# Optimization experiments

Measured on AMD Instinct MI355X. Metric: run time of the kernel, lower is better.

The kernel has to match this reference:

```python
import jax, jax.numpy as jnp
import numpy as np

B, T, I, H = 512, 64, 128, 128
E = I - 1  # encoder_in


def _cell(x, h, c, Wih, Whh, bih, bhh):
    # PyTorch LSTM gate order: i, f, g, o
    g = x @ Wih.T + h @ Whh.T + bih + bhh
    i, f, gg, o = jnp.split(g, 4, axis=-1)
    c2 = jax.nn.sigmoid(f) * c + jax.nn.sigmoid(i) * jnp.tanh(gg)
    h2 = jax.nn.sigmoid(o) * jnp.tanh(c2)
    return h2, c2


def setup_inputs() -> dict:
    key = jax.random.key(0)
    ks = iter(jax.random.split(key, 40))
    n = lambda *s: jax.random.normal(next(ks), s, dtype=jnp.float32) * 0.05
    inp = {
        'input_data': jax.random.normal(next(ks), (B, T, I), dtype=jnp.float32),
        # encoder LSTM (2 layers, input E)
        'enc_Wih0': n(4 * H, E), 'enc_Whh0': n(4 * H, H), 'enc_bih0': n(4 * H), 'enc_bhh0': n(4 * H),
        'enc_Wih1': n(4 * H, H), 'enc_Whh1': n(4 * H, H), 'enc_bih1': n(4 * H), 'enc_bhh1': n(4 * H),
        # decoder LSTM (2 layers, input 1)
        'dec_Wih0': n(4 * H, 1), 'dec_Whh0': n(4 * H, H), 'dec_bih0': n(4 * H), 'dec_bhh0': n(4 * H),
        'dec_Wih1': n(4 * H, H), 'dec_Whh1': n(4 * H, H), 'dec_bih1': n(4 * H), 'dec_bhh1': n(4 * H),
        # input attention MLP: (2H+T)->T->1
        'attn_W1': n(T, 2 * H + T), 'attn_b1': n(T), 'attn_W2': n(1, T), 'attn_b2': n(1),
        # temporal attention MLP: 3H->H->1
        'attnd_W1': n(H, 3 * H), 'attnd_b1': n(H), 'attnd_W2': n(1, H), 'attnd_b2': n(1),
        # decoder input projection (H+1)->1 and output projection 2H->1
        'decin_W': n(1, H + 1), 'decin_b': n(1),
        'proj_W': n(1, 2 * H), 'proj_b': n(1),
    }
    return inp


def reference(input_data, enc_Wih0, enc_Whh0, enc_bih0, enc_bhh0,
              enc_Wih1, enc_Whh1, enc_bih1, enc_bhh1,
              dec_Wih0, dec_Whh0, dec_bih0, dec_bhh0,
              dec_Wih1, dec_Whh1, dec_bih1, dec_bhh1,
              attn_W1, attn_b1, attn_W2, attn_b2,
              attnd_W1, attnd_b1, attnd_W2, attnd_b2,
              decin_W, decin_b, proj_W, proj_b):
    b, t, i = input_data.shape
    e, hdim = i - 1, enc_Whh0.shape[1]
    inp_enc = input_data[:, :, 1:]              # [B,T,E]
    inp_dec = input_data[:, :, 0]               # [B,T]
    inp_perm = jnp.transpose(inp_enc, (0, 2, 1))  # [B,E,T]
    z = jnp.zeros((b, hdim), input_data.dtype)

    def enc_step(carry, x_t):
        h0, c0, h1, c1 = carry
        hc = jnp.concatenate([
            jnp.broadcast_to(h1[:, None, :], (b, e, hdim)),
            jnp.broadcast_to(c1[:, None, :], (b, e, hdim)),
            inp_perm], axis=-1)                              # [B,E,2H+T]
        logits = jnp.tanh(hc @ attn_W1.T + attn_b1) @ attn_W2.T + attn_b2
        a = jax.nn.softmax(logits[..., 0], axis=-1)          # [B,E]
        h0, c0 = _cell(x_t * a, h0, c0, enc_Wih0, enc_Whh0, enc_bih0, enc_bhh0)
        h1, c1 = _cell(h0, h1, c1, enc_Wih1, enc_Whh1, enc_bih1, enc_bhh1)
        return (h0, c0, h1, c1), h1

    _, h_top = jax.lax.scan(enc_step, (z, z, z, z), jnp.transpose(inp_enc, (1, 0, 2)))
    h_exp = jnp.transpose(h_top, (1, 0, 2))  # [B,T,H]

    def dec_step(carry, x_t):
        h0, c0, h1, c1, _ = carry
        hc = jnp.concatenate([
            jnp.broadcast_to(h1[:, None, :], (b, t, hdim)),
            jnp.broadcast_to(c1[:, None, :], (b, t, hdim)),
            h_exp], axis=-1)                                  # [B,T,3H]
        logits = jnp.tanh(hc @ attnd_W1.T + attnd_b1) @ attnd_W2.T + attnd_b2
        a = jax.nn.softmax(logits[..., 0], axis=-1)           # [B,T]
        partial = jnp.einsum('bth,bt->bh', h_exp, a)          # [B,H]
        full = jnp.concatenate([partial, x_t[:, None]], axis=-1)  # [B,H+1]
        din = full @ decin_W.T + decin_b                      # [B,1]
        h0, c0 = _cell(din, h0, c0, dec_Wih0, dec_Whh0, dec_bih0, dec_bhh0)
        h1, c1 = _cell(h0, h1, c1, dec_Wih1, dec_Whh1, dec_bih1, dec_bhh1)
        return (h0, c0, h1, c1, partial), None

    (h0, c0, h1, c1, partial), _ = jax.lax.scan(dec_step, (z, z, z, z, z), jnp.transpose(inp_dec))
    out = jnp.concatenate([h1, partial], axis=-1) @ proj_W.T + proj_b  # [B,1]
    return out
```

## Files before the change

### kernel.cpp

```cpp
#include <hip/hip_runtime.h>

#define BATCH 512
#define TT 64
#define II 128

#define OFF_Wr_e0 0
#define OFF_Wr_e1 (OFF_Wr_e0 + 512*256)
#define OFF_Wr_d1 (OFF_Wr_e1 + 512*256)
#define OFF_bs0e  (OFF_Wr_d1 + 512*256)
#define OFF_bs1e  (OFF_bs0e + 512)
#define OFF_bs0d  (OFF_bs1e + 512)
#define OFF_bs1d  (OFF_bs0d + 512)
#define OFF_xprojT (OFF_bs1d + 512)
#define OFF_hexp   (OFF_xprojT + BATCH*8192)
#define OFF_hprojT (OFF_hexp + BATCH*8192)

struct Params {
  const float* input;
  const float *eWih0, *eWhh0, *ebih0, *ebhh0, *eWih1, *eWhh1, *ebih1, *ebhh1;
  const float *dWih0, *dWhh0, *dbih0, *dbhh0, *dWih1, *dWhh1, *dbih1, *dbhh1;
  const float *aW1, *ab1, *aW2, *ab2;
  const float *adW1, *adb1, *adW2, *adb2;
  const float *dinW, *dinb, *projW, *projb;
  float* ws;
  float* out;
};

#define L2E 1.4426950408889634f

__device__ __forceinline__ float exp2f_(float x){ return __builtin_amdgcn_exp2f(x); }
__device__ __forceinline__ float rcp_(float x){ return __builtin_amdgcn_rcpf(x); }
__device__ __forceinline__ float fast_tanh(float x){
  float t = exp2f_(x * 2.8853900817779268f);
  return 1.f - 2.f * rcp_(t + 1.f);
}
__device__ __forceinline__ float sigm(float x){
  return rcp_(1.f + exp2f_(-x * L2E));
}
__device__ __forceinline__ float wave_max(float v){
  #pragma unroll
  for (int o = 32; o > 0; o >>= 1) v = fmaxf(v, __shfl_xor(v, o, 64));
  return v;
}
__device__ __forceinline__ float wave_sum(float v){
  #pragma unroll
  for (int o = 32; o > 0; o >>= 1) v += __shfl_xor(v, o, 64);
  return v;
}

__global__ __launch_bounds__(256) void k_prep(Params p){
  float* ws = p.ws;
  const int gid = blockIdx.x*256 + threadIdx.x;
  const int gsz = gridDim.x*256;
  for (int i = gid; i < 512*256; i += gsz){
    const int j = i >> 8, k = i & 255;
    ws[OFF_Wr_e0 + i] = (k < 128) ? ((k < 127) ? p.eWih0[j*127 + k] : 0.f)
                                  : p.eWhh0[j*128 + (k-128)];
    ws[OFF_Wr_e1 + i] = (k < 128) ? p.eWih1[j*128 + k] : p.eWhh1[j*128 + (k-128)];
    ws[OFF_Wr_d1 + i] = (k < 128) ? p.dWih1[j*128 + k] : p.dWhh1[j*128 + (k-128)];
  }
  for (int i = gid; i < 512; i += gsz){
    ws[OFF_bs0e+i] = p.ebih0[i]+p.ebhh0[i];
    ws[OFF_bs1e+i] = p.ebih1[i]+p.ebhh1[i];
    ws[OFF_bs0d+i] = p.dbih0[i]+p.dbhh0[i];
    ws[OFF_bs1d+i] = p.dbih1[i]+p.dbhh1[i];
  }
}

__global__ __launch_bounds__(256) void k_xproj(Params p){
  __shared__ float xin[64][128];
  __shared__ float w1x[64][64];
  __shared__ float b1s[64];
  const int b = blockIdx.x, tid = threadIdx.x;
  const float* inb = p.input + (size_t)b*(TT*II);
  for (int i = tid; i < 64*128; i += 256){
    const int k = i >> 7, e = i & 127;
    xin[k][e] = (e < 127) ? inb[k*II + 1 + e] : 0.f;
  }
  for (int i = tid; i < 64*64; i += 256){
    const int j = i >> 6, k = i & 63;
    w1x[j][k] = p.aW1[j*320 + 256 + k];
  }
  if (tid < 64) b1s[tid] = p.ab1[tid];
  __syncthreads();
  float* outb = p.ws + OFF_xprojT + (size_t)b*8192;
  for (int i = tid; i < 64*128; i += 256){
    const int j = i >> 7, e = i & 127;
    float acc = b1s[j];
    #pragma unroll 8
    for (int k = 0; k < 64; ++k) acc += xin[k][e] * w1x[j][k];
    outb[i] = acc;
  }
}

__global__ __launch_bounds__(256) void k_hproj(Params p){
  __shared__ float hx[64][129];
  __shared__ float bs[128];
  const int b = blockIdx.x, tid = threadIdx.x;
  const float* hb = p.ws + OFF_hexp + (size_t)b*8192;
  for (int i = tid; i < 64*128; i += 256){
    hx[i>>7][i&127] = hb[i];
  }
  if (tid < 128) bs[tid] = p.adb1[tid];
  __syncthreads();
  float* outb = p.ws + OFF_hprojT + (size_t)b*8192;
  for (int i = tid; i < 128*64; i += 256){
    const int kk = i >> 6, t2 = i & 63;
    const float* w = p.adW1 + kk*384 + 256;
    float acc = bs[kk];
    #pragma unroll 8
    for (int k = 0; k < 128; ++k) acc += hx[t2][k] * w[k];
    outb[i] = acc;
  }
}

#define ENC_LDS_FLOATS 40784
__global__ __launch_bounds__(1024, 4) void k_enc(Params p){
  extern __shared__ float sm[];
  float* xp  = sm;
  float* Se  = xp + 32768;
  float* c0  = Se + 2048;
  float* gpA = c0 + 512;
  float* gpB = gpA + 2048;
  float* scr = gpB + 2048;
  float* g01 = scr + 1024;
  float* w2  = g01 + 256;
  float* pm  = w2 + 64;
  float* psu = pm + 8;
  const int tid = threadIdx.x;
  const int b0 = blockIdx.x * 4;
  float* ws = p.ws;

  {
    const float4* xsrc = (const float4*)(ws + OFF_xprojT + (size_t)b0*8192);
    float4* xdst = (float4*)xp;
    for (int i = tid; i < 8192; i += 1024) xdst[i] = xsrc[i];
  }
  for (int i = tid; i < 2048; i += 1024) Se[i] = 0.f;
  if (tid < 512) c0[tid] = 0.f;
  if (tid < 64) w2[tid] = p.aW2[tid];
  const float b2 = p.ab2[0];
  const int j = tid & 511, kh = tid >> 9;
  const float bias0 = ws[OFF_bs0e + j];
  const float bias1 = ws[OFF_bs1e + j];
  const int jj = tid & 63, bb1 = (tid>>6)&3, kq = tid >> 8;
  const int e2 = tid & 127, bb2 = (tid>>7)&3, jh = tid >> 9;
  const int hf = (tid>>6)&1;
  __syncthreads();

  for (int t = 0; t < TT; ++t){
    {
      const float4* wr = (const float4*)(p.aW1 + jj*320 + kq*64);
      const float4* s1 = (const float4*)(Se + bb1*512 + 256 + kq*64);
      float a = 0.f;
      #pragma unroll 8
      for (int g = 0; g < 16; ++g){
        const float4 w = wr[g], x = s1[g];
        a += w.x*x.x + w.y*x.y + w.z*x.z + w.w*x.w;
      }
      scr[kq*256 + bb1*64 + jj] = a;
    }
    __syncthreads();
    if (tid < 256) g01[tid] = scr[tid] + scr[256+tid] + scr[512+tid] + scr[768+tid];
    __syncthreads();
    {
      const float* xpe = xp + bb2*8192 + e2;
      const float* gg = g01 + bb2*64 + jh*32;
      const float* w2p = w2 + jh*32;
      float acc = 0.f;
      #pragma unroll 8
      for (int q = 0; q < 32; ++q)
        acc += w2p[q] * fast_tanh(xpe[(jh*32+q)*128] + gg[q]);
      scr[jh*512 + bb2*128 + e2] = acc;
    }
    __syncthreads();
    float acc_l;
    {
      acc_l = scr[bb2*128 + e2] + scr[512 + bb2*128 + e2] + b2;
      if (e2 == 127) acc_l = -3.0e38f;
      const float m = wave_max(acc_l);
      const float pe = exp2f_((acc_l - m)*L2E);
      const float s = wave_sum(pe);
      if ((tid & 63) == 0){ pm[bb2*2+hf] = m; psu[bb2*2+hf] = s; }
    }
    __syncthreads();
    {
      const float m0 = pm[bb2*2], m1 = pm[bb2*2+1];
      const float gm = fmaxf(m0, m1);
      const float tot = psu[bb2*2]*exp2f_((m0-gm)*L2E) + psu[bb2*2+1]*exp2f_((m1-gm)*L2E);
      const float a = exp2f_((acc_l - gm)*L2E) * rcp_(tot);
      float xv = 0.f;
      if (e2 < 127) xv = p.input[(size_t)(b0+bb2)*8192 + t*128 + 1 + e2] * a;
      Se[bb2*512 + e2] = xv;
    }
    __syncthreads();
    {
      const float4* r  = (const float4*)(ws + OFF_Wr_e0 + (j<<8) + (kh<<7));
      const float4* x0 = (const float4*)(Se + (kh<<7));
      const float4* x1 = (const float4*)(Se + 512 + (kh<<7));
      const float4* x2 = (const float4*)(Se + 1024 + (kh<<7));
      const float4* x3 = (const float4*)(Se + 1536 + (kh<<7));
      float a0,a1,a2,a3; a0=a1=a2=a3 = kh ? 0.f : bias0;
      #pragma unroll 8
      for (int kg = 0; kg < 32; ++kg){
        const float4 w = r[kg];
        const float4 v0=x0[kg], v1=x1[kg], v2=x2[kg], v3=x3[kg];
        a0 += w.x*v0.x + w.y*v0.y + w.z*v0.z + w.w*v0.w;
        a1 += w.x*v1.x + w.y*v1.y + w.z*v1.z + w.w*v1.w;
        a2 += w.x*v2.x + w.y*v2.y + w.z*v2.z + w.w*v2.w;
        a3 += w.x*v3.x + w.y*v3.y + w.z*v3.z + w.w*v3.w;
      }
      float* gp = kh ? gpB : gpA;
      gp[j] = a0; gp[512+j] = a1; gp[1024+j] = a2; gp[1536+j] = a3;
    }
    __syncthreads();
    if (tid < 512){
      const int bb = tid>>7, u = tid&127;
      const float* gA = gpA + bb*512; const float* gB = gpB + bb*512;
      const float gi = gA[u]+gB[u], gf = gA[128+u]+gB[128+u];
      const float gg2 = gA[256+u]+gB[256+u], go = gA[384+u]+gB[384+u];
      const float c = sigm(gf)*c0[tid] + sigm(gi)*fast_tanh(gg2);
      c0[tid] = c;
      Se[bb*512 + 128 + u] = sigm(go)*fast_tanh(c);
    }
    __syncthreads();
    {
      const float4* r  = (const float4*)(ws + OFF_Wr_e1 + (j<<8) + (kh<<7));
      const float4* x0 = (const float4*)(Se + 128 + (kh<<7));
      const float4* x1 = (const float4*)(Se + 640 + (kh<<7));
      const float4* x2 = (const float4*)(Se + 1152 + (kh<<7));
      const float4* x3 = (const float4*)(Se + 1664 + (kh<<7));
      float a0,a1,a2,a3; a0=a1=a2=a3 = kh ? 0.f : bias1;
      #pragma unroll 8
      for (int kg = 0; kg < 32; ++kg){
        const float4 w = r[kg];
        const float4 v0=x0[kg], v1=x1[kg], v2=x2[kg], v3=x3[kg];
        a0 += w.x*v0.x + w.y*v0.y + w.z*v0.z + w.w*v0.w;
        a1 += w.x*v1.x + w.y*v1.y + w.z*v1.z + w.w*v1.w;
        a2 += w.x*v2.x + w.y*v2.y + w.z*v2.z + w.w*v2.w;
        a3 += w.x*v3.x + w.y*v3.y + w.z*v3.z + w.w*v3.w;
      }
      float* gp = kh ? gpB : gpA;
      gp[j] = a0; gp[512+j] = a1; gp[1024+j] = a2; gp[1536+j] = a3;
    }
    __syncthreads();
    if (tid < 512){
      const int bb = tid>>7, u = tid&127;
      const float* gA = gpA + bb*512; const float* gB = gpB + bb*512;
      const float gi = gA[u]+gB[u], gf = gA[128+u]+gB[128+u];
      const float gg2 = gA[256+u]+gB[256+u], go = gA[384+u]+gB[384+u];
      const float c = sigm(gf)*Se[bb*512+384+u] + sigm(gi)*fast_tanh(gg2);
      Se[bb*512+384+u] = c;
      const float h = sigm(go)*fast_tanh(c);
      Se[bb*512+256+u] = h;
      ws[OFF_hexp + (size_t)(b0+bb)*8192 + t*128 + u] = h;
    }
    __syncthreads();
  }
}

#define DEC_LDS_FLOATS 40584
__global__ __launch_bounds__(1024, 4) void k_dec(Params p){
  extern __shared__ float sm[];
  float* hp  = sm;
  float* Sd  = hp + 32768;
  float* c0  = Sd + 1536;
  float* gpA = c0 + 512;
  float* gpB = gpA + 2048;
  float* scr = gpB + 2048;
  float* g01 = scr + 1024;
  float* wd2 = g01 + 512;
  float* dins= wd2 + 128;
  const int tid = threadIdx.x;
  const int b0 = blockIdx.x * 4;
  float* ws = p.ws;

  {
    const float4* hsrc = (const float4*)(ws + OFF_hprojT + (size_t)b0*8192);
    float4* hdst = (float4*)hp;
    for (int i = tid; i < 8192; i += 1024) hdst[i] = hsrc[i];
  }
  for (int i = tid; i < 1536; i += 1024) Sd[i] = 0.f;
  if (tid < 512) c0[tid] = 0.f;
  if (tid < 128) wd2[tid] = p.adW2[tid];
  const int j = tid & 511, kh = tid >> 9;
  const float bias0d = ws[OFF_bs0d + j];
  const float bias1d = ws[OFF_bs1d + j];
  const float dW0j = p.dWih0[j];
  const int o = tid & 511, bbD = o>>7, kkD = o&127;
  const int l = tid & 63, wv = tid >> 6;
  const int bbA = wv>>2, kqA = wv&3;
  const int th = tid>>9, bbC = (tid>>7)&3, hC = tid&127;
  const float dinw0 = p.dinW[l], dinw1 = p.dinW[64+l];
  const float dinw128 = p.dinW[128], dinbv = p.dinb[0];
  const float bd2 = p.adb2[0];
  const float pw0 = p.projW[l], pw1 = p.projW[64+l];
  const float pw2 = p.projW[128+l], pw3 = p.projW[192+l];
  const float pb = p.projb[0];
  __syncthreads();

  for (int t = 0; t < TT; ++t){
    {
      const float4* wr = (const float4*)(p.adW1 + kkD*384 + (kh<<7));
      const float4* sx = (const float4*)(Sd + bbD*384 + 128 + (kh<<7));
      float a = 0.f;
      #pragma unroll 8
      for (int kg = 0; kg < 32; ++kg){
        const float4 w = wr[kg], x = sx[kg];
        a += w.x*x.x + w.y*x.y + w.z*x.z + w.w*x.w;
      }
      (kh ? gpB : gpA)[o] = a;
    }
    __syncthreads();
    g01[tid&511] = gpA[tid&511] + gpB[tid&511];
    __syncthreads();
    {
      const float* hpb = hp + bbA*8192 + l;
      const float* gg = g01 + bbA*128 + kqA*32;
      const float* w2p = wd2 + kqA*32;
      float acc = 0.f;
      #pragma unroll 8
      for (int q = 0; q < 32; ++q)
        acc += w2p[q] * fast_tanh(hpb[(kqA*32+q)*64] + gg[q]);
      scr[kqA*256 + bbA*64 + l] = acc;
    }
    __syncthreads();
    {
      const int q = tid & 255;
      float acc = scr[q] + scr[256+q] + scr[512+q] + scr[768+q] + bd2;
      const float m = wave_max(acc);
      const float pe = exp2f_((acc - m)*L2E);
      const float s = wave_sum(pe);
      g01[q] = pe * rcp_(s);
    }
    __syncthreads();
    {
      const float* he = ws + OFF_hexp + (size_t)(b0+bbC)*8192 + hC;
      const float* av = g01 + bbC*64 + th*32;
      float acc = 0.f;
      #pragma unroll 8
      for (int q = 0; q < 32; ++q)
        acc += av[q] * he[(th*32+q)*128];
      (th ? gpB : gpA)[bbC*128 + hC] = acc;
    }
    __syncthreads();
    scr[tid&511] = gpA[tid&511] + gpB[tid&511];
    __syncthreads();
    if (wv < 4){
      float v = scr[wv*128 + l]*dinw0 + scr[wv*128 + 64 + l]*dinw1;
      v = wave_sum(v);
      if (l == 0){
        const float xd = p.input[(size_t)(b0+wv)*8192 + t*128];
        dins[wv] = v + xd*dinw128 + dinbv;
      }
    }
    __syncthreads();
    {
      const float4* wr = (const float4*)(p.dWhh0 + (j<<7) + (kh<<6));
      const float4* x0 = (const float4*)(Sd + (kh<<6));
      const float4* x1 = (const float4*)(Sd + 384 + (kh<<6));
      const float4* x2 = (const float4*)(Sd + 768 + (kh<<6));
      const float4* x3 = (const float4*)(Sd + 1152 + (kh<<6));
      float a0,a1,a2,a3;
      if (kh){ a0=a1=a2=a3=0.f; }
      else {
        a0 = bias0d + dins[0]*dW0j; a1 = bias0d + dins[1]*dW0j;
        a2 = bias0d + dins[2]*dW0j; a3 = bias0d + dins[3]*dW0j;
      }
      #pragma unroll 8
      for (int kg = 0; kg < 16; ++kg){
        const float4 w = wr[kg];
        const float4 v0=x0[kg], v1=x1[kg], v2=x2[kg], v3=x3[kg];
        a0 += w.x*v0.x + w.y*v0.y + w.z*v0.z + w.w*v0.w;
        a1 += w.x*v1.x + w.y*v1.y + w.z*v1.z + w.w*v1.w;
        a2 += w.x*v2.x + w.y*v2.y + w.z*v2.z + w.w*v2.w;
        a3 += w.x*v3.x + w.y*v3.y + w.z*v3.z + w.w*v3.w;
      }
      float* gp = kh ? gpB : gpA;
      gp[j] = a0; gp[512+j] = a1; gp[1024+j] = a2; gp[1536+j] = a3;
    }
    __syncthreads();
    if (tid < 512){
      const int bb = tid>>7, u = tid&127;
      const float* gA = gpA + bb*512; const float* gB = gpB + bb*512;
      const float gi = gA[u]+gB[u], gf = gA[128+u]+gB[128+u];
      const float gg2 = gA[256+u]+gB[256+u], go = gA[384+u]+gB[384+u];
      const float c = sigm(gf)*c0[tid] + sigm(gi)*fast_tanh(gg2);
      c0[tid] = c;
      Sd[bb*384 + u] = sigm(go)*fast_tanh(c);
    }
    __syncthreads();
    {
      const float4* wr = (const float4*)(ws + OFF_Wr_d1 + (j<<8) + (kh<<7));
      const float4* x0 = (const float4*)(Sd + (kh<<7));
      const float4* x1 = (const float4*)(Sd + 384 + (kh<<7));
      const float4* x2 = (const float4*)(Sd + 768 + (kh<<7));
      const float4* x3 = (const float4*)(Sd + 1152 + (kh<<7));
      float a0,a1,a2,a3; a0=a1=a2=a3 = kh ? 0.f : bias1d;
      #pragma unroll 8
      for (int kg = 0; kg < 32; ++kg){
        const float4 w = wr[kg];
        const float4 v0=x0[kg], v1=x1[kg], v2=x2[kg], v3=x3[kg];
        a0 += w.x*v0.x + w.y*v0.y + w.z*v0.z + w.w*v0.w;
        a1 += w.x*v1.x + w.y*v1.y + w.z*v1.z + w.w*v1.w;
        a2 += w.x*v2.x + w.y*v2.y + w.z*v2.z + w.w*v2.w;
        a3 += w.x*v3.x + w.y*v3.y + w.z*v3.z + w.w*v3.w;
      }
      float* gp = kh ? gpB : gpA;
      gp[j] = a0; gp[512+j] = a1; gp[1024+j] = a2; gp[1536+j] = a3;
    }
    __syncthreads();
    if (tid < 512){
      const int bb = tid>>7, u = tid&127;
      const float* gA = gpA + bb*512; const float* gB = gpB + bb*512;
      const float gi = gA[u]+gB[u], gf = gA[128+u]+gB[128+u];
      const float gg2 = gA[256+u]+gB[256+u], go = gA[384+u]+gB[384+u];
      const float c = sigm(gf)*Sd[bb*384+256+u] + sigm(gi)*fast_tanh(gg2);
      Sd[bb*384+256+u] = c;
      Sd[bb*384+128+u] = sigm(go)*fast_tanh(c);
    }
    __syncthreads();
  }
  if (wv < 4){
    float v = Sd[wv*384+128+l]*pw0 + Sd[wv*384+192+l]*pw1
            + scr[wv*128+l]*pw2 + scr[wv*128+64+l]*pw3;
    v = wave_sum(v);
    if (l == 0) p.out[b0 + wv] = v + pb;
  }
}

extern "C" void kernel_launch(void* const* d_in, const int* in_sizes, int n_in,
                              void* d_out, int out_size, void* d_ws, size_t ws_size,
                              hipStream_t stream){
  Params p;
  p.input = (const float*)d_in[0];
  p.eWih0=(const float*)d_in[1];  p.eWhh0=(const float*)d_in[2];
  p.ebih0=(const float*)d_in[3];  p.ebhh0=(const float*)d_in[4];
  p.eWih1=(const float*)d_in[5];  p.eWhh1=(const float*)d_in[6];
  p.ebih1=(const float*)d_in[7];  p.ebhh1=(const float*)d_in[8];
  p.dWih0=(const float*)d_in[9];  p.dWhh0=(const float*)d_in[10];
  p.dbih0=(const float*)d_in[11]; p.dbhh0=(const float*)d_in[12];
  p.dWih1=(const float*)d_in[13]; p.dWhh1=(const float*)d_in[14];
  p.dbih1=(const float*)d_in[15]; p.dbhh1=(const float*)d_in[16];
  p.aW1=(const float*)d_in[17];   p.ab1=(const float*)d_in[18];
  p.aW2=(const float*)d_in[19];   p.ab2=(const float*)d_in[20];
  p.adW1=(const float*)d_in[21];  p.adb1=(const float*)d_in[22];
  p.adW2=(const float*)d_in[23];  p.adb2=(const float*)d_in[24];
  p.dinW=(const float*)d_in[25];  p.dinb=(const float*)d_in[26];
  p.projW=(const float*)d_in[27]; p.projb=(const float*)d_in[28];
  p.ws = (float*)d_ws;
  p.out = (float*)d_out;

  (void)hipFuncSetAttribute(reinterpret_cast<const void*>(k_enc),
      hipFuncAttributeMaxDynamicSharedMemorySize, ENC_LDS_FLOATS*4);
  (void)hipFuncSetAttribute(reinterpret_cast<const void*>(k_dec),
      hipFuncAttributeMaxDynamicSharedMemorySize, DEC_LDS_FLOATS*4);

  hipLaunchKernelGGL(k_prep,  dim3(128), dim3(256), 0, stream, p);
  hipLaunchKernelGGL(k_xproj, dim3(BATCH), dim3(256), 0, stream, p);
  hipLaunchKernelGGL(k_enc,   dim3(128), dim3(1024), ENC_LDS_FLOATS*4, stream, p);
  hipLaunchKernelGGL(k_hproj, dim3(BATCH), dim3(256), 0, stream, p);
  hipLaunchKernelGGL(k_dec,   dim3(128), dim3(1024), DEC_LDS_FLOATS*4, stream, p);
}
```

Baseline: 5.658 ms.

## Restructure encoder/decoder recurrence to cut barriers and reductions via wave shuffles

Thread-to-work mappings in the recurrent encoder and decoder kernels are remapped so partial dot-product sums are combined with intra-wave shuffles instead of LDS scratch passes. This removes several block-wide barriers per timestep. __syncthreads is replaced with a custom lgkmcnt wait plus s_barrier. The first weight vectors are prefetched into registers, the decoder's projected-history tile gets a padded LDS layout, and hexp is written with nontemporal stores. The cost is higher register pressure, and the custom barrier only waits on LDS and scalar-memory (lgkmcnt) operations, not on outstanding global loads.

New measurement: 5.655 ms. No clear change (-0.1%).

```diff
diff --git a/kernel.cpp b/kernel.cpp
--- a/kernel.cpp
+++ b/kernel.cpp
@@ -47,6 +47,15 @@
   for (int o = 32; o > 0; o >>= 1) v += __shfl_xor(v, o, 64);
   return v;
 }
+__device__ __forceinline__ void bar_lds(){
+  asm volatile("s_waitcnt lgkmcnt(0)\n\ts_barrier" ::: "memory");
+}
+
+#define FMA4(W,V0,V1,V2,V3) \
+  a0 += (W).x*(V0).x + (W).y*(V0).y + (W).z*(V0).z + (W).w*(V0).w; \
+  a1 += (W).x*(V1).x + (W).y*(V1).y + (W).z*(V1).z + (W).w*(V1).w; \
+  a2 += (W).x*(V2).x + (W).y*(V2).y + (W).z*(V2).z + (W).w*(V2).w; \
+  a3 += (W).x*(V3).x + (W).y*(V3).y + (W).z*(V3).z + (W).w*(V3).w;
 
 __global__ __launch_bounds__(256) void k_prep(Params p){
   float* ws = p.ws;
@@ -98,9 +107,7 @@
   __shared__ float bs[128];
   const int b = blockIdx.x, tid = threadIdx.x;
   const float* hb = p.ws + OFF_hexp + (size_t)b*8192;
-  for (int i = tid; i < 64*128; i += 256){
-    hx[i>>7][i&127] = hb[i];
-  }
+  for (int i = tid; i < 64*128; i += 256) hx[i>>7][i&127] = hb[i];
   if (tid < 128) bs[tid] = p.adb1[tid];
   __syncthreads();
   float* outb = p.ws + OFF_hprojT + (size_t)b*8192;
@@ -114,318 +121,313 @@
   }
 }
 
-#define ENC_LDS_FLOATS 40784
+#define ENC_LDS_FLOATS 39776
 __global__ __launch_bounds__(1024, 4) void k_enc(Params p){
   extern __shared__ float sm[];
-  float* xp  = sm;
-  float* Se  = xp + 32768;
-  float* c0  = Se + 2048;
-  float* gpA = c0 + 512;
-  float* gpB = gpA + 2048;
-  float* scr = gpB + 2048;
-  float* g01 = scr + 1024;
-  float* w2  = g01 + 256;
-  float* pm  = w2 + 64;
-  float* psu = pm + 8;
+  float* xp   = sm;
+  float* Se   = xp + 32768;
+  float* c0s  = Se + 2048;
+  float* gpA  = c0s + 512;
+  float* gpB  = gpA + 2048;
+  float* g01s = gpB + 2048;
+  float* w2   = g01s + 256;
+  float* pm   = w2 + 64;
+  float* psu  = pm + 16;
   const int tid = threadIdx.x;
-  const int b0 = blockIdx.x * 4;
+  const int b0 = blockIdx.x*4;
   float* ws = p.ws;
 
-  {
-    const float4* xsrc = (const float4*)(ws + OFF_xprojT + (size_t)b0*8192);
+  { const float4* xsrc = (const float4*)(ws + OFF_xprojT + (size_t)b0*8192);
     float4* xdst = (float4*)xp;
-    for (int i = tid; i < 8192; i += 1024) xdst[i] = xsrc[i];
-  }
+    for (int i = tid; i < 8192; i += 1024) xdst[i] = xsrc[i]; }
   for (int i = tid; i < 2048; i += 1024) Se[i] = 0.f;
-  if (tid < 512) c0[tid] = 0.f;
+  if (tid < 512) c0s[tid] = 0.f;
   if (tid < 64) w2[tid] = p.aW2[tid];
   const float b2 = p.ab2[0];
-  const int j = tid & 511, kh = tid >> 9;
-  const float bias0 = ws[OFF_bs0e + j];
-  const float bias1 = ws[OFF_bs1e + j];
-  const int jj = tid & 63, bb1 = (tid>>6)&3, kq = tid >> 8;
-  const int e2 = tid & 127, bb2 = (tid>>7)&3, jh = tid >> 9;
-  const int hf = (tid>>6)&1;
+
+  const int bbW = tid >> 8;
+  const int wvq = (tid >> 6) & 3;
+  const int kqE = tid & 3, oE = tid >> 2, jjE = oE & 63;
+  const int jhE = tid & 1, eE = (tid >> 1) & 127;
+  const int jG = tid & 511, khG = tid >> 9;
+  const float bias0 = ws[OFF_bs0e + jG];
+  const float bias1 = ws[OFF_bs1e + jG];
+  const float4* wE1 = (const float4*)(p.aW1 + jjE*320 + kqE*64);
+  const float4* wE3 = (const float4*)(ws + OFF_Wr_e0 + (jG<<8) + (khG<<7));
+  const float4* wE4 = (const float4*)(ws + OFF_Wr_e1 + (jG<<8) + (khG<<7));
+  const float* xrow = p.input + (size_t)(b0+bbW)*8192 + 1 + eE;
+  float4 pfE1[4], pfE3[4], pfE4[4];
+  #pragma unroll
+  for (int i = 0; i < 4; ++i){ pfE1[i]=wE1[i]; pfE3[i]=wE3[i]; pfE4[i]=wE4[i]; }
   __syncthreads();
 
   for (int t = 0; t < TT; ++t){
     {
-      const float4* wr = (const float4*)(p.aW1 + jj*320 + kq*64);
-      const float4* s1 = (const float4*)(Se + bb1*512 + 256 + kq*64);
+      const float4* s1 = (const float4*)(Se + bbW*512 + 256 + kqE*64);
+      float a = 0.f;
+      #pragma unroll
+      for (int kg = 0; kg < 4; ++kg){ float4 w = pfE1[kg], x = s1[kg];
+        a += w.x*x.x + w.y*x.y + w.z*x.z + w.w*x.w; }
+      #pragma unroll
+      for (int kg = 4; kg < 16; ++kg){ float4 w = wE1[kg], x = s1[kg];
+        a += w.x*x.x + w.y*x.y + w.z*x.z + w.w*x.w; }
+      a += __shfl_xor(a, 1, 64);
+      a += __shfl_xor(a, 2, 64);
+      if (kqE == 0) g01s[oE] = a;
+    }
+    bar_lds();
+    float accL;
+    {
+      const float* xpe = xp + bbW*8192 + eE;
+      const float* gg = g01s + bbW*64 + jhE*32;
+      const float* w2p = w2 + jhE*32;
       float a = 0.f;
       #pragma unroll 8
-      for (int g = 0; g < 16; ++g){
-        const float4 w = wr[g], x = s1[g];
-        a += w.x*x.x + w.y*x.y + w.z*x.z + w.w*x.w;
-      }
-      scr[kq*256 + bb1*64 + jj] = a;
-    }
-    __syncthreads();
-    if (tid < 256) g01[tid] = scr[tid] + scr[256+tid] + scr[512+tid] + scr[768+tid];
-    __syncthreads();
-    {
-      const float* xpe = xp + bb2*8192 + e2;
-      const float* gg = g01 + bb2*64 + jh*32;
-      const float* w2p = w2 + jh*32;
-      float acc = 0.f;
-      #pragma unroll 8
       for (int q = 0; q < 32; ++q)
-        acc += w2p[q] * fast_tanh(xpe[(jh*32+q)*128] + gg[q]);
-      scr[jh*512 + bb2*128 + e2] = acc;
-    }
-    __syncthreads();
-    float acc_l;
-    {
-      acc_l = scr[bb2*128 + e2] + scr[512 + bb2*128 + e2] + b2;
-      if (e2 == 127) acc_l = -3.0e38f;
-      const float m = wave_max(acc_l);
-      const float pe = exp2f_((acc_l - m)*L2E);
-      const float s = wave_sum(pe);
-      if ((tid & 63) == 0){ pm[bb2*2+hf] = m; psu[bb2*2+hf] = s; }
-    }
-    __syncthreads();
-    {
-      const float m0 = pm[bb2*2], m1 = pm[bb2*2+1];
-      const float gm = fmaxf(m0, m1);
-      const float tot = psu[bb2*2]*exp2f_((m0-gm)*L2E) + psu[bb2*2+1]*exp2f_((m1-gm)*L2E);
-      const float a = exp2f_((acc_l - gm)*L2E) * rcp_(tot);
+        a += w2p[q] * fast_tanh(xpe[(jhE*32+q)*128] + gg[q]);
+      a += __shfl_xor(a, 1, 64);
+      a += b2;
+      if (eE == 127) a = -3.0e38f;
+      accL = a;
+      const float m = wave_max(a);
+      const float pe = exp2f_((a - m)*L2E);
+      const float s = wave_sum(pe)*0.5f;
+      if ((tid & 63) == 0){ pm[bbW*4+wvq] = m; psu[bbW*4+wvq] = s; }
+    }
+    bar_lds();
+    {
+      const float m0=pm[bbW*4],m1=pm[bbW*4+1],m2=pm[bbW*4+2],m3=pm[bbW*4+3];
+      const float gm = fmaxf(fmaxf(m0,m1),fmaxf(m2,m3));
+      const float tot = psu[bbW*4]*exp2f_((m0-gm)*L2E) + psu[bbW*4+1]*exp2f_((m1-gm)*L2E)
+                      + psu[bbW*4+2]*exp2f_((m2-gm)*L2E) + psu[bbW*4+3]*exp2f_((m3-gm)*L2E);
+      const float a = exp2f_((accL-gm)*L2E)*rcp_(tot);
       float xv = 0.f;
-      if (e2 < 127) xv = p.input[(size_t)(b0+bb2)*8192 + t*128 + 1 + e2] * a;
-      Se[bb2*512 + e2] = xv;
-    }
-    __syncthreads();
-    {
-      const float4* r  = (const float4*)(ws + OFF_Wr_e0 + (j<<8) + (kh<<7));
-      const float4* x0 = (const float4*)(Se + (kh<<7));
-      const float4* x1 = (const float4*)(Se + 512 + (kh<<7));
-      const float4* x2 = (const float4*)(Se + 1024 + (kh<<7));
-      const float4* x3 = (const float4*)(Se + 1536 + (kh<<7));
-      float a0,a1,a2,a3; a0=a1=a2=a3 = kh ? 0.f : bias0;
-      #pragma unroll 8
-      for (int kg = 0; kg < 32; ++kg){
-        const float4 w = r[kg];
-        const float4 v0=x0[kg], v1=x1[kg], v2=x2[kg], v3=x3[kg];
-        a0 += w.x*v0.x + w.y*v0.y + w.z*v0.z + w.w*v0.w;
-        a1 += w.x*v1.x + w.y*v1.y + w.z*v1.z + w.w*v1.w;
-        a2 += w.x*v2.x + w.y*v2.y + w.z*v2.z + w.w*v2.w;
-        a3 += w.x*v3.x + w.y*v3.y + w.z*v3.z + w.w*v3.w;
-      }
-      float* gp = kh ? gpB : gpA;
-      gp[j] = a0; gp[512+j] = a1; gp[1024+j] = a2; gp[1536+j] = a3;
-    }
-    __syncthreads();
+      if (eE < 127) xv = xrow[t*128] * a;
+      Se[bbW*512 + eE] = xv;
+    }
+    bar_lds();
+    {
+      float a0,a1,a2,a3; a0=a1=a2=a3 = khG ? 0.f : bias0;
+      const float4* x0 = (const float4*)(Se + (khG<<7));
+      const float4* x1 = x0 + 128; const float4* x2 = x0 + 256; const float4* x3 = x0 + 384;
+      #pragma unroll
+      for (int kg = 0; kg < 4; ++kg){ float4 w = pfE3[kg];
+        float4 v0=x0[kg],v1=x1[kg],v2=x2[kg],v3=x3[kg]; FMA4(w,v0,v1,v2,v3) }
+      #pragma unroll 7
+      for (int kg = 4; kg < 32; ++kg){ float4 w = wE3[kg];
+        float4 v0=x0[kg],v1=x1[kg],v2=x2[kg],v3=x3[kg]; FMA4(w,v0,v1,v2,v3) }
+      float* gp = khG ? gpB : gpA;
+      gp[jG]=a0; gp[512+jG]=a1; gp[1024+jG]=a2; gp[1536+jG]=a3;
+    }
+    bar_lds();
     if (tid < 512){
       const int bb = tid>>7, u = tid&127;
       const float* gA = gpA + bb*512; const float* gB = gpB + bb*512;
-      const float gi = gA[u]+gB[u], gf = gA[128+u]+gB[128+u];
-      const float gg2 = gA[256+u]+gB[256+u], go = gA[384+u]+gB[384+u];
-      const float c = sigm(gf)*c0[tid] + sigm(gi)*fast_tanh(gg2);
-      c0[tid] = c;
+      const float gi=gA[u]+gB[u], gf=gA[128+u]+gB[128+u];
+      const float gg2=gA[256+u]+gB[256+u], go=gA[384+u]+gB[384+u];
+      const float c = sigm(gf)*c0s[tid] + sigm(gi)*fast_tanh(gg2);
+      c0s[tid] = c;
       Se[bb*512 + 128 + u] = sigm(go)*fast_tanh(c);
     }
-    __syncthreads();
-    {
-      const float4* r  = (const float4*)(ws + OFF_Wr_e1 + (j<<8) + (kh<<7));
-      const float4* x0 = (const float4*)(Se + 128 + (kh<<7));
-      const float4* x1 = (const float4*)(Se + 640 + (kh<<7));
-      const float4* x2 = (const float4*)(Se + 1152 + (kh<<7));
-      const float4* x3 = (const float4*)(Se + 1664 + (kh<<7));
-      float a0,a1,a2,a3; a0=a1=a2=a3 = kh ? 0.f : bias1;
-      #pragma unroll 8
-      for (int kg = 0; kg < 32; ++kg){
-        const float4 w = r[kg];
-        const float4 v0=x0[kg], v1=x1[kg], v2=x2[kg], v3=x3[kg];
-        a0 += w.x*v0.x + w.y*v0.y + w.z*v0.z + w.w*v0.w;
-        a1 += w.x*v1.x + w.y*v1.y + w.z*v1.z + w.w*v1.w;
-        a2 += w.x*v2.x + w.y*v2.y + w.z*v2.z + w.w*v2.w;
-        a3 += w.x*v3.x + w.y*v3.y + w.z*v3.z + w.w*v3.w;
-      }
-      float* gp = kh ? gpB : gpA;
-      gp[j] = a0; gp[512+j] = a1; gp[1024+j] = a2; gp[1536+j] = a3;
-    }
-    __syncthreads();
+    bar_lds();
+    {
+      float a0,a1,a2,a3; a0=a1=a2=a3 = khG ? 0.f : bias1;
+      const float4* x0 = (const float4*)(Se + 128 + (khG<<7));
+      const float4* x1 = x0 + 128; const float4* x2 = x0 + 256; const float4* x3 = x0 + 384;
+      #pragma unroll
+      for (int kg = 0; kg < 4; ++kg){ float4 w = pfE4[kg];
+        float4 v0=x0[kg],v1=x1[kg],v2=x2[kg],v3=x3[kg]; FMA4(w,v0,v1,v2,v3) }
+      #pragma unroll 7
+      for (int kg = 4; kg < 32; ++kg){ float4 w = wE4[kg];
+        float4 v0=x0[kg],v1=x1[kg],v2=x2[kg],v3=x3[kg]; FMA4(w,v0,v1,v2,v3) }
+      float* gp = khG ? gpB : gpA;
+      gp[jG]=a0; gp[512+jG]=a1; gp[1024+jG]=a2; gp[1536+jG]=a3;
+    }
+    bar_lds();
     if (tid < 512){
       const int bb = tid>>7, u = tid&127;
       const float* gA = gpA + bb*512; const float* gB = gpB + bb*512;
-      const float gi = gA[u]+gB[u], gf = gA[128+u]+gB[128+u];
-      const float gg2 = gA[256+u]+gB[256+u], go = gA[384+u]+gB[384+u];
+      const float gi=gA[u]+gB[u], gf=gA[128+u]+gB[128+u];
+      const float gg2=gA[256+u]+gB[256+u], go=gA[384+u]+gB[384+u];
       const float c = sigm(gf)*Se[bb*512+384+u] + sigm(gi)*fast_tanh(gg2);
       Se[bb*512+384+u] = c;
       const float h = sigm(go)*fast_tanh(c);
       Se[bb*512+256+u] = h;
-      ws[OFF_hexp + (size_t)(b0+bb)*8192 + t*128 + u] = h;
-    }
-    __syncthreads();
-  }
-}
-
-#define DEC_LDS_FLOATS 40584
+      __builtin_nontemporal_store(h, ws + OFF_hexp + (size_t)(b0+bb)*8192 + t*128 + u);
+    }
+    bar_lds();
+  }
+}
+
+#define DEC_LDS_FLOATS 40880
 __global__ __launch_bounds__(1024, 4) void k_dec(Params p){
   extern __shared__ float sm[];
-  float* hp  = sm;
-  float* Sd  = hp + 32768;
-  float* c0  = Sd + 1536;
-  float* gpA = c0 + 512;
-  float* gpB = gpA + 2048;
-  float* scr = gpB + 2048;
-  float* g01 = scr + 1024;
-  float* wd2 = g01 + 512;
-  float* dins= wd2 + 128;
+  float* hp    = sm;
+  float* Sd    = hp + 33280;
+  float* c0s   = Sd + 1536;
+  float* gpA   = c0s + 512;
+  float* gpB   = gpA + 2048;
+  float* parts = gpB + 2048;
+  float* g01d  = parts + 512;
+  float* lraw  = g01d + 512;
+  float* pm    = lraw + 256;
+  float* psu   = pm + 16;
+  float* dpart = psu + 16;
+  float* wd2   = dpart + 16;
   const int tid = threadIdx.x;
-  const int b0 = blockIdx.x * 4;
+  const int b0 = blockIdx.x*4;
   float* ws = p.ws;
 
-  {
-    const float4* hsrc = (const float4*)(ws + OFF_hprojT + (size_t)b0*8192);
-    float4* hdst = (float4*)hp;
-    for (int i = tid; i < 8192; i += 1024) hdst[i] = hsrc[i];
-  }
+  { const float* hsrc = ws + OFF_hprojT + (size_t)b0*8192;
+    for (int i = tid; i < 32768; i += 1024){
+      const int bb = i>>13, kk = (i>>6)&127, tl = i&63;
+      hp[bb*8320 + kk*65 + tl] = hsrc[i];
+    } }
   for (int i = tid; i < 1536; i += 1024) Sd[i] = 0.f;
-  if (tid < 512) c0[tid] = 0.f;
+  if (tid < 512) c0s[tid] = 0.f;
   if (tid < 128) wd2[tid] = p.adW2[tid];
-  const int j = tid & 511, kh = tid >> 9;
-  const float bias0d = ws[OFF_bs0d + j];
-  const float bias1d = ws[OFF_bs1d + j];
-  const float dW0j = p.dWih0[j];
-  const int o = tid & 511, bbD = o>>7, kkD = o&127;
-  const int l = tid & 63, wv = tid >> 6;
-  const int bbA = wv>>2, kqA = wv&3;
-  const int th = tid>>9, bbC = (tid>>7)&3, hC = tid&127;
-  const float dinw0 = p.dinW[l], dinw1 = p.dinW[64+l];
+  const float bd2 = p.adb2[0];
+
+  const int bbW = tid >> 8, wvq = (tid >> 6) & 3;
+  const int khD = tid & 1, kkD = (tid >> 1) & 127;
+  const int kq4 = tid & 3, o4 = tid >> 2, tl4 = o4 & 63;
+  const int thC = tid & 1, hC = (tid >> 1) & 127;
+  const int jG = tid & 511, khG = tid >> 9;
+  const float bias0d = ws[OFF_bs0d + jG];
+  const float bias1d = ws[OFF_bs1d + jG];
+  const float dW0j = p.dWih0[jG];
+  const float dinw_h = p.dinW[hC];
   const float dinw128 = p.dinW[128], dinbv = p.dinb[0];
-  const float bd2 = p.adb2[0];
-  const float pw0 = p.projW[l], pw1 = p.projW[64+l];
-  const float pw2 = p.projW[128+l], pw3 = p.projW[192+l];
-  const float pb = p.projb[0];
+  const float4* wD1 = (const float4*)(p.adW1 + kkD*384 + khD*128);
+  const float4* wD3 = (const float4*)(p.dWhh0 + (jG<<7) + (khG<<6));
+  const float4* wD4 = (const float4*)(ws + OFF_Wr_d1 + (jG<<8) + (khG<<7));
+  const float* heB = ws + OFF_hexp + (size_t)(b0+bbW)*8192 + thC*4096 + hC;
+  float4 pfD1[4], pfD3[4], pfD4[4];
+  #pragma unroll
+  for (int i = 0; i < 4; ++i){ pfD1[i]=wD1[i]; pfD3[i]=wD3[i]; pfD4[i]=wD4[i]; }
   __syncthreads();
 
   for (int t = 0; t < TT; ++t){
     {
-      const float4* wr = (const float4*)(p.adW1 + kkD*384 + (kh<<7));
-      const float4* sx = (const float4*)(Sd + bbD*384 + 128 + (kh<<7));
+      const float4* sx = (const float4*)(Sd + bbW*384 + 128 + khD*128);
+      float a = 0.f;
+      #pragma unroll
+      for (int kg = 0; kg < 4; ++kg){ float4 w = pfD1[kg], x = sx[kg];
+        a += w.x*x.x + w.y*x.y + w.z*x.z + w.w*x.w; }
+      #pragma unroll 7
+      for (int kg = 4; kg < 32; ++kg){ float4 w = wD1[kg], x = sx[kg];
+        a += w.x*x.x + w.y*x.y + w.z*x.z + w.w*x.w; }
+      a += __shfl_xor(a, 1, 64);
+      if (khD == 0) g01d[bbW*128 + kkD] = a;
+    }
+    bar_lds();
+    float lacc;
+    {
+      const float* hpb = hp + bbW*8320 + tl4;
+      const float* gg = g01d + bbW*128;
       float a = 0.f;
       #pragma unroll 8
-      for (int kg = 0; kg < 32; ++kg){
-        const float4 w = wr[kg], x = sx[kg];
-        a += w.x*x.x + w.y*x.y + w.z*x.z + w.w*x.w;
+      for (int q = 0; q < 32; ++q){
+        const int kk = q*4 + kq4;
+        a += wd2[kk] * fast_tanh(hpb[kk*65] + gg[kk]);
       }
-      (kh ? gpB : gpA)[o] = a;
-    }
-    __syncthreads();
-    g01[tid&511] = gpA[tid&511] + gpB[tid&511];
-    __syncthreads();
-    {
-      const float* hpb = hp + bbA*8192 + l;
-      const float* gg = g01 + bbA*128 + kqA*32;
-      const float* w2p = wd2 + kqA*32;
-      float acc = 0.f;
+      a += __shfl_xor(a, 1, 64);
+      a += __shfl_xor(a, 2, 64);
+      a += bd2;
+      lacc = a;
+      if (kq4 == 0) lraw[o4] = a;
+      const float m = wave_max(a);
+      const float pe = exp2f_((a-m)*L2E);
+      const float s = wave_sum(pe)*0.25f;
+      if ((tid&63)==0){ pm[bbW*4+wvq]=m; psu[bbW*4+wvq]=s; }
+    }
+    bar_lds();
+    if (tid < 256){
+      const int bb = tid>>6;
+      const float m0=pm[bb*4],m1=pm[bb*4+1],m2=pm[bb*4+2],m3=pm[bb*4+3];
+      const float gm = fmaxf(fmaxf(m0,m1),fmaxf(m2,m3));
+      const float tot = psu[bb*4]*exp2f_((m0-gm)*L2E)+psu[bb*4+1]*exp2f_((m1-gm)*L2E)
+                      +psu[bb*4+2]*exp2f_((m2-gm)*L2E)+psu[bb*4+3]*exp2f_((m3-gm)*L2E);
+      lraw[tid] = exp2f_((lraw[tid]-gm)*L2E)*rcp_(tot);
+    }
+    bar_lds();
+    {
+      const float* av = lraw + bbW*64 + thC*32;
+      float a = 0.f;
       #pragma unroll 8
-      for (int q = 0; q < 32; ++q)
-        acc += w2p[q] * fast_tanh(hpb[(kqA*32+q)*64] + gg[q]);
-      scr[kqA*256 + bbA*64 + l] = acc;
-    }
-    __syncthreads();
-    {
-      const int q = tid & 255;
-      float acc = scr[q] + scr[256+q] + scr[512+q] + scr[768+q] + bd2;
-      const float m = wave_max(acc);
-      const float pe = exp2f_((acc - m)*L2E);
-      const float s = wave_sum(pe);
-      g01[q] = pe * rcp_(s);
-    }
-    __syncthreads();
-    {
-      const float* he = ws + OFF_hexp + (size_t)(b0+bbC)*8192 + hC;
-      const float* av = g01 + bbC*64 + th*32;
-      float acc = 0.f;
-      #pragma unroll 8
-      for (int q = 0; q < 32; ++q)
-        acc += av[q] * he[(th*32+q)*128];
-      (th ? gpB : gpA)[bbC*128 + hC] = acc;
-    }
-    __syncthreads();
-    scr[tid&511] = gpA[tid&511] + gpB[tid&511];
-    __syncthreads();
-    if (wv < 4){
-      float v = scr[wv*128 + l]*dinw0 + scr[wv*128 + 64 + l]*dinw1;
-      v = wave_sum(v);
-      if (l == 0){
-        const float xd = p.input[(size_t)(b0+wv)*8192 + t*128];
-        dins[wv] = v + xd*dinw128 + dinbv;
-      }
-    }
-    __syncthreads();
-    {
-      const float4* wr = (const float4*)(p.dWhh0 + (j<<7) + (kh<<6));
-      const float4* x0 = (const float4*)(Sd + (kh<<6));
-      const float4* x1 = (const float4*)(Sd + 384 + (kh<<6));
-      const float4* x2 = (const float4*)(Sd + 768 + (kh<<6));
-      const float4* x3 = (const float4*)(Sd + 1152 + (kh<<6));
+      for (int q = 0; q < 32; ++q) a += av[q] * heB[q*128];
+      a += __shfl_xor(a, 1, 64);
+      if (thC == 0) parts[bbW*128 + hC] = a;
+      float v = a * dinw_h;
+      v = wave_sum(v)*0.5f;
+      if ((tid&63)==0) dpart[bbW*4+wvq] = v;
+    }
+    bar_lds();
+    {
+      const float xd0 = p.input[(size_t)(b0+0)*8192 + t*128];
+      const float xd1 = p.input[(size_t)(b0+1)*8192 + t*128];
+      const float xd2 = p.input[(size_t)(b0+2)*8192 + t*128];
+      const float xd3 = p.input[(size_t)(b0+3)*8192 + t*128];
+      const float dn0 = dpart[0]+dpart[1]+dpart[2]+dpart[3] + xd0*dinw128 + dinbv;
+      const float dn1 = dpart[4]+dpart[5]+dpart[6]+dpart[7] + xd1*dinw128 + dinbv;
+      const float dn2 = dpart[8]+dpart[9]+dpart[10]+dpart[11] + xd2*dinw128 + dinbv;
+      const float dn3 = dpart[12]+dpart[13]+dpart[14]+dpart[15] + xd3*dinw128 + dinbv;
       float a0,a1,a2,a3;
-      if (kh){ a0=a1=a2=a3=0.f; }
-      else {
-        a0 = bias0d + dins[0]*dW0j; a1 = bias0d + dins[1]*dW0j;
-        a2 = bias0d + dins[2]*dW0j; a3 = bias0d + dins[3]*dW0j;
-      }
-      #pragma unroll 8
-      for (int kg = 0; kg < 16; ++kg){
-        const float4 w = wr[kg];
-        const float4 v0=x0[kg], v1=x1[kg], v2=x2[kg], v3=x3[kg];
-        a0 += w.x*v0.x + w.y*v0.y + w.z*v0.z + w.w*v0.w;
-        a1 += w.x*v1.x + w.y*v1.y + w.z*v1.z + w.w*v1.w;
-        a2 += w.x*v2.x + w.y*v2.y + w.z*v2.z + w.w*v2.w;
-        a3 += w.x*v3.x + w.y*v3.y + w.z*v3.z + w.w*v3.w;
-      }
-      float* gp = kh ? gpB : gpA;
-      gp[j] = a0; gp[512+j] = a1; gp[1024+j] = a2; gp[1536+j] = a3;
-    }
-    __syncthreads();
+      if (khG){ a0=a1=a2=a3=0.f; }
+      else { a0=bias0d+dn0*dW0j; a1=bias0d+dn1*dW0j; a2=bias0d+dn2*dW0j; a3=bias0d+dn3*dW0j; }
+      const float4* x0 = (const float4*)(Sd + (khG<<6));
+      const float4* x1 = x0 + 96; const float4* x2 = x0 + 192; const float4* x3 = x0 + 288;
+      #pragma unroll
+      for (int kg = 0; kg < 4; ++kg){ float4 w = pfD3[kg];
+        float4 v0=x0[kg],v1=x1[kg],v2=x2[kg],v3=x3[kg]; FMA4(w,v0,v1,v2,v3) }
+      #pragma unroll
+      for (int kg = 4; kg < 16; ++kg){ float4 w = wD3[kg];
+        float4 v0=x0[kg],v1=x1[kg],v2=x2[kg],v3=x3[kg]; FMA4(w,v0,v1,v2,v3) }
+      float* gp = khG ? gpB : gpA;
+      gp[jG]=a0; gp[512+jG]=a1; gp[1024+jG]=a2; gp[1536+jG]=a3;
+    }
+    bar_lds();
     if (tid < 512){
       const int bb = tid>>7, u = tid&127;
       const float* gA = gpA + bb*512; const float* gB = gpB + bb*512;
-      const float gi = gA[u]+gB[u], gf = gA[128+u]+gB[128+u];
-      const float gg2 = gA[256+u]+gB[256+u], go = gA[384+u]+gB[384+u];
-      const float c = sigm(gf)*c0[tid] + sigm(gi)*fast_tanh(gg2);
-      c0[tid] = c;
+      const float gi=gA[u]+gB[u], gf=gA[128+u]+gB[128+u];
+      const float gg2=gA[256+u]+gB[256+u], go=gA[384+u]+gB[384+u];
+      const float c = sigm(gf)*c0s[tid] + sigm(gi)*fast_tanh(gg2);
+      c0s[tid] = c;
       Sd[bb*384 + u] = sigm(go)*fast_tanh(c);
     }
-    __syncthreads();
-    {
-      const float4* wr = (const float4*)(ws + OFF_Wr_d1 + (j<<8) + (kh<<7));
-      const float4* x0 = (const float4*)(Sd + (kh<<7));
-      const float4* x1 = (const float4*)(Sd + 384 + (kh<<7));
-      const float4* x2 = (const float4*)(Sd + 768 + (kh<<7));
-      const float4* x3 = (const float4*)(Sd + 1152 + (kh<<7));
-      float a0,a1,a2,a3; a0=a1=a2=a3 = kh ? 0.f : bias1d;
-      #pragma unroll 8
-      for (int kg = 0; kg < 32; ++kg){
-        const float4 w = wr[kg];
-        const float4 v0=x0[kg], v1=x1[kg], v2=x2[kg], v3=x3[kg];
-        a0 += w.x*v0.x + w.y*v0.y + w.z*v0.z + w.w*v0.w;
-        a1 += w.x*v1.x + w.y*v1.y + w.z*v1.z + w.w*v1.w;
-        a2 += w.x*v2.x + w.y*v2.y + w.z*v2.z + w.w*v2.w;
-        a3 += w.x*v3.x + w.y*v3.y + w.z*v3.z + w.w*v3.w;
-      }
-      float* gp = kh ? gpB : gpA;
-      gp[j] = a0; gp[512+j] = a1; gp[1024+j] = a2; gp[1536+j] = a3;
-    }
-    __syncthreads();
+    bar_lds();
+    {
+      float a0,a1,a2,a3; a0=a1=a2=a3 = khG ? 0.f : bias1d;
+      const float4* x0 = (const float4*)(Sd + (khG<<7));
+      const float4* x1 = x0 + 96; const float4* x2 = x0 + 192; const float4* x3 = x0 + 288;
+      #pragma unroll
+      for (int kg = 0; kg < 4; ++kg){ float4 w = pfD4[kg];
+        float4 v0=x0[kg],v1=x1[kg],v2=x2[kg],v3=x3[kg]; FMA4(w,v0,v1,v2,v3) }
+      #pragma unroll 7
+      for (int kg = 4; kg < 32; ++kg){ float4 w = wD4[kg];
+        float4 v0=x0[kg],v1=x1[kg],v2=x2[kg],v3=x3[kg]; FMA4(w,v0,v1,v2,v3) }
+      float* gp = khG ? gpB : gpA;
+      gp[jG]=a0; gp[512+jG]=a1; gp[1024+jG]=a2; gp[1536+jG]=a3;
+    }
+    bar_lds();
     if (tid < 512){
       const int bb = tid>>7, u = tid&127;
       const float* gA = gpA + bb*512; const float* gB = gpB + bb*512;
-      const float gi = gA[u]+gB[u], gf = gA[128+u]+gB[128+u];
-      const float gg2 = gA[256+u]+gB[256+u], go = gA[384+u]+gB[384+u];
+      const float gi=gA[u]+gB[u], gf=gA[128+u]+gB[128+u];
+      const float gg2=gA[256+u]+gB[256+u], go=gA[384+u]+gB[384+u];
       const float c = sigm(gf)*Sd[bb*384+256+u] + sigm(gi)*fast_tanh(gg2);
       Sd[bb*384+256+u] = c;
       Sd[bb*384+128+u] = sigm(go)*fast_tanh(c);
     }
-    __syncthreads();
-  }
-  if (wv < 4){
-    float v = Sd[wv*384+128+l]*pw0 + Sd[wv*384+192+l]*pw1
-            + scr[wv*128+l]*pw2 + scr[wv*128+64+l]*pw3;
+    bar_lds();
+  }
+  if (tid < 256){
+    const int bb = tid>>6, l = tid&63;
+    float v = Sd[bb*384+128+l]*p.projW[l] + Sd[bb*384+192+l]*p.projW[64+l]
+            + parts[bb*128+l]*p.projW[128+l] + parts[bb*128+64+l]*p.projW[192+l];
     v = wave_sum(v);
-    if (l == 0) p.out[b0 + wv] = v + pb;
+    if (l == 0) p.out[b0 + bb] = v + p.projb[0];
   }
 }
 
```
